# Optimization experiments

Measured on AMD Instinct MI355X. Metric: run time of the kernel, lower is better.

The kernel has to match this reference:

```python
import jax, jax.numpy as jnp
import numpy as np

B, N, DX, DZ = 16384, 128, 5, 2
R_DIAG = 0.1

def setup_inputs() -> dict:
    key = jax.random.key(0)
    ks = jax.random.split(key, 8)
    inp = {
        'state_old': jax.random.normal(ks[0], (B, N, DX), jnp.float32),
        'y': jax.random.normal(ks[1], (B, N, DZ), jnp.float32),
        'encoding': jax.random.normal(ks[2], (B, 128), jnp.float32),
        'pw1': jax.random.normal(ks[3], (2, 16), jnp.float32) * (1.0 / np.sqrt(2.0)),
        'pb1': jnp.zeros((16,), jnp.float32),
        'pw2': jax.random.normal(ks[4], (16, 32), jnp.float32) * (1.0 / np.sqrt(16.0)),
        'pb2': jnp.zeros((32,), jnp.float32),
        'pw3': jax.random.normal(ks[5], (32, 2), jnp.float32) * (1.0 / np.sqrt(32.0)),
        'pb3': jnp.zeros((2,), jnp.float32),
        'nw1': jax.random.normal(ks[6], (128, 32), jnp.float32) * (1.0 / np.sqrt(128.0)),
        'nb1': jnp.zeros((32,), jnp.float32),
        'nw2': jax.random.normal(ks[7], (32, 2), jnp.float32) * (1.0 / np.sqrt(32.0)),
        'nb2': jnp.zeros((2,), jnp.float32),
        # ObservationNoise build(): learned bias init = sqrt(r_diag^2 - 0.001), fixed bias init = 0.001
        'learned_obs_bias': jnp.full((DZ,), float(np.sqrt(R_DIAG**2 - 0.001)), jnp.float32),
        'fixed_obs_bias': jnp.full((DZ,), 0.001, jnp.float32),
    }
    return inp

def _process_model(state, pw1, pb1, pw2, pb2, pw3, pb3):
    # state: [B*N, 5] -> nonlinear unicycle propagation + learned residual on [v, theta_dot]
    theta = state[:, 2] + state[:, 4]
    v = state[:, 3]
    theta_dot = state[:, 4]
    x = state[:, 0] + v * jnp.sin(theta)
    y = state[:, 1] + v * jnp.cos(theta)
    data_in = jnp.stack([v, theta_dot], axis=-1)  # [B*N, 2]
    h = jax.nn.relu(data_in @ pw1 + pb1)
    h = jax.nn.relu(h @ pw2 + pb2)
    data_out = data_in + (h @ pw3 + pb3)
    return jnp.concatenate([x[:, None], y[:, None], theta[:, None], data_out], axis=-1)

def reference(state_old, y, encoding, pw1, pb1, pw2, pb2, pw3, pb3,
              nw1, nb1, nw2, nb2, learned_obs_bias, fixed_obs_bias):
    b, n, dx = state_old.shape
    dz = y.shape[-1]
    # --- predict step: propagate every ensemble member through the process model ---
    Xp = _process_model(state_old.reshape(b * n, dx), pw1, pb1, pw2, pb2, pw3, pb3)
    Xp = Xp.reshape(b, n, dx)
    # --- observation model: H picks state dims 3,4 (H = [[0,0,0,1,0],[0,0,0,0,1]]) ---
    HX = Xp[..., 3:5]  # [b, n, dz]
    # --- observation noise R (heteroscedastic diag) from encoding ---
    d = jax.nn.relu(encoding @ nw1 + nb1) @ nw2 + nb2  # [b, dz]
    diag = jnp.square(d + learned_obs_bias) + fixed_obs_bias
    R = jnp.eye(dz, dtype=diag.dtype) * diag[:, None, :]  # [b, dz, dz]
    # --- ensemble statistics ---
    A = Xp - Xp.mean(axis=1, keepdims=True)    # state anomalies [b, n, dx]
    HA = HX - HX.mean(axis=1, keepdims=True)   # obs anomalies   [b, n, dz]
    denom = jnp.asarray(n - 1, Xp.dtype)
    Pzz = jnp.einsum('bnz,bnw->bzw', HA, HA) / denom + R  # [b, dz, dz]
    Pxz = jnp.einsum('bnx,bnz->bxz', A, HA) / denom       # [b, dx, dz]
    # Kalman gain K = Pxz @ inv(Pzz); compute K^T via batched solve
    Kt = jnp.linalg.solve(Pzz, jnp.swapaxes(Pxz, 1, 2))   # [b, dz, dx]
    innovation = y - HX                                   # [b, n, dz]
    X_new = Xp + jnp.einsum('bnz,bzx->bnx', innovation, Kt)
    return X_new
```

## Files before the change

kernel.cpp:

```cpp
#include <hip/hip_runtime.h>


#define NBPB 4

typedef __bf16 bf16x8 __attribute__((ext_vector_type(8)));
typedef float  f32x16 __attribute__((ext_vector_type(16)));

__global__ __launch_bounds__(256) void ekf_fused(
    const float* __restrict__ state_old,
    const float* __restrict__ y_obs,
    const float* __restrict__ encoding,
    const float* __restrict__ pw1,
    const float* __restrict__ pb1,
    const float* __restrict__ pw2,
    const float* __restrict__ pb2,
    const float* __restrict__ pw3,
    const float* __restrict__ pb3,
    const float* __restrict__ nw1,
    const float* __restrict__ nb1,
    const float* __restrict__ nw2,
    const float* __restrict__ nb2,
    const float* __restrict__ lob,
    const float* __restrict__ fob,
    float* __restrict__ out)
{
    __shared__ __align__(16) float s_state[NBPB * 640];

    const int t = threadIdx.x;
    const int base = blockIdx.x * NBPB;

    {
        const float4* src = (const float4*)(state_old + (size_t)base * 640);
        float4* dst = (float4*)s_state;
        #pragma unroll
        for (int i = t; i < NBPB * 160; i += 256) dst[i] = src[i];
    }
    __syncthreads();

    const int w = t >> 6;
    const int l = t & 63;
    const int c = l & 31;
    const int h = l >> 5;
    const size_t b = (size_t)base + w;

    float diag0, diag1;
    {
        const float4* eg4 = (const float4*)(encoding + b * 128) + h * 16;
        const float* wp = nw1 + (size_t)(h * 64) * 32 + c;
        float a0 = 0.f, a1 = 0.f, a2 = 0.f, a3 = 0.f;
        #pragma unroll
        for (int kk = 0; kk < 16; ++kk) {
            float4 e4 = eg4[kk];
            a0 = fmaf(e4.x, wp[(4 * kk + 0) * 32], a0);
            a1 = fmaf(e4.y, wp[(4 * kk + 1) * 32], a1);
            a2 = fmaf(e4.z, wp[(4 * kk + 2) * 32], a2);
            a3 = fmaf(e4.w, wp[(4 * kk + 3) * 32], a3);
        }
        float acc = (a0 + a1) + (a2 + a3);
        acc += __shfl_xor(acc, 32, 64);
        acc += nb1[c];
        float hh = fmaxf(acc, 0.f);
        float d0 = hh * nw2[2 * c + 0];
        float d1 = hh * nw2[2 * c + 1];
        #pragma unroll
        for (int off = 1; off < 32; off <<= 1) {
            d0 += __shfl_xor(d0, off, 64);
            d1 += __shfl_xor(d1, off, 64);
        }
        float e0 = d0 + nb2[0] + lob[0];
        float e1 = d1 + nb2[1] + lob[1];
        diag0 = fmaf(e0, e0, fob[0]);
        diag1 = fmaf(e1, e1, fob[1]);
    }

    const float4 pw1a0 = *(const float4*)(pw1 + 8 * h);
    const float4 pw1a1 = *(const float4*)(pw1 + 8 * h + 4);
    const float4 pw1b0 = *(const float4*)(pw1 + 16 + 8 * h);
    const float4 pw1b1 = *(const float4*)(pw1 + 16 + 8 * h + 4);
    const float4 pb1k0 = *(const float4*)(pb1 + 8 * h);
    const float4 pb1k1 = *(const float4*)(pb1 + 8 * h + 4);
    float4 pb2v[4], pw3lo[4], pw3hi[4];
    #pragma unroll
    for (int gr = 0; gr < 4; ++gr) {
        pb2v[gr]  = *(const float4*)(pb2 + 8 * gr + 4 * h);
        pw3lo[gr] = *(const float4*)(pw3 + 16 * gr + 8 * h);
        pw3hi[gr] = *(const float4*)(pw3 + 16 * gr + 8 * h + 4);
    }
    bf16x8 afrag;
    #pragma unroll
    for (int q = 0; q < 8; ++q)
        afrag[q] = (__bf16)pw2[(8 * h + q) * 32 + c];
    f32x16 cinit;
    #pragma unroll
    for (int gr = 0; gr < 4; ++gr) {
        cinit[4 * gr + 0] = pb2v[gr].x;
        cinit[4 * gr + 1] = pb2v[gr].y;
        cinit[4 * gr + 2] = pb2v[gr].z;
        cinit[4 * gr + 3] = pb2v[gr].w;
    }

    const float* sp = s_state + w * 640;
    float o3m[4], o4m[4];
    #pragma unroll
    for (int m = 0; m < 4; ++m) {
        const float* s5 = sp + (c + 32 * m) * 5;
        float v = s5[3], td = s5[4];
        bf16x8 bfrag;
        bfrag[0] = (__bf16)fmaxf(0.f, fmaf(v, pw1a0.x, fmaf(td, pw1b0.x, pb1k0.x)));
        bfrag[1] = (__bf16)fmaxf(0.f, fmaf(v, pw1a0.y, fmaf(td, pw1b0.y, pb1k0.y)));
        bfrag[2] = (__bf16)fmaxf(0.f, fmaf(v, pw1a0.z, fmaf(td, pw1b0.z, pb1k0.z)));
        bfrag[3] = (__bf16)fmaxf(0.f, fmaf(v, pw1a0.w, fmaf(td, pw1b0.w, pb1k0.w)));
        bfrag[4] = (__bf16)fmaxf(0.f, fmaf(v, pw1a1.x, fmaf(td, pw1b1.x, pb1k1.x)));
        bfrag[5] = (__bf16)fmaxf(0.f, fmaf(v, pw1a1.y, fmaf(td, pw1b1.y, pb1k1.y)));
        bfrag[6] = (__bf16)fmaxf(0.f, fmaf(v, pw1a1.z, fmaf(td, pw1b1.z, pb1k1.z)));
        bfrag[7] = (__bf16)fmaxf(0.f, fmaf(v, pw1a1.w, fmaf(td, pw1b1.w, pb1k1.w)));
        f32x16 acc = __builtin_amdgcn_mfma_f32_32x32x16_bf16(afrag, bfrag, cinit, 0, 0, 0);
        float o3 = 0.f, o4 = 0.f;
        #pragma unroll
        for (int gr = 0; gr < 4; ++gr) {
            float r0 = fmaxf(acc[4 * gr + 0], 0.f);
            float r1 = fmaxf(acc[4 * gr + 1], 0.f);
            float r2 = fmaxf(acc[4 * gr + 2], 0.f);
            float r3 = fmaxf(acc[4 * gr + 3], 0.f);
            o3 = fmaf(r0, pw3lo[gr].x, o3); o4 = fmaf(r0, pw3lo[gr].y, o4);
            o3 = fmaf(r1, pw3lo[gr].z, o3); o4 = fmaf(r1, pw3lo[gr].w, o4);
            o3 = fmaf(r2, pw3hi[gr].x, o3); o4 = fmaf(r2, pw3hi[gr].y, o4);
            o3 = fmaf(r3, pw3hi[gr].z, o3); o4 = fmaf(r3, pw3hi[gr].w, o4);
        }
        o3m[m] = o3; o4m[m] = o4;
    }
    #pragma unroll
    for (int m = 0; m < 4; ++m) {
        o3m[m] += __shfl_xor(o3m[m], 32, 64);
        o4m[m] += __shfl_xor(o4m[m], 32, 64);
    }

    const float pb30 = pb3[0], pb31 = pb3[1];
    float o3s0 = h ? o3m[2] : o3m[0];
    float o3s1 = h ? o3m[3] : o3m[1];
    float o4s0 = h ? o4m[2] : o4m[0];
    float o4s1 = h ? o4m[3] : o4m[1];
    float xpo[2][5];
    #pragma unroll
    for (int mm = 0; mm < 2; ++mm) {
        const float* s5 = sp + (c + 32 * (2 * h + mm)) * 5;
        float s0 = s5[0], s1 = s5[1], s2 = s5[2], v = s5[3], td = s5[4];
        float th = s2 + td;
        xpo[mm][0] = fmaf(v, __sinf(th), s0);
        xpo[mm][1] = fmaf(v, __cosf(th), s1);
        xpo[mm][2] = th;
        xpo[mm][3] = v  + (mm ? o3s1 : o3s0) + pb30;
        xpo[mm][4] = td + (mm ? o4s1 : o4s0) + pb31;
    }

    float red[14];
    #pragma unroll
    for (int i = 0; i < 5; ++i) red[i] = xpo[0][i] + xpo[1][i];
    red[5]  = xpo[0][0] * xpo[0][3] + xpo[1][0] * xpo[1][3];
    red[6]  = xpo[0][0] * xpo[0][4] + xpo[1][0] * xpo[1][4];
    red[7]  = xpo[0][1] * xpo[0][3] + xpo[1][1] * xpo[1][3];
    red[8]  = xpo[0][1] * xpo[0][4] + xpo[1][1] * xpo[1][4];
    red[9]  = xpo[0][2] * xpo[0][3] + xpo[1][2] * xpo[1][3];
    red[10] = xpo[0][2] * xpo[0][4] + xpo[1][2] * xpo[1][4];
    red[11] = xpo[0][3] * xpo[0][3] + xpo[1][3] * xpo[1][3];
    red[12] = xpo[0][3] * xpo[0][4] + xpo[1][3] * xpo[1][4];
    red[13] = xpo[0][4] * xpo[0][4] + xpo[1][4] * xpo[1][4];
    #pragma unroll
    for (int off = 1; off < 64; off <<= 1) {
        #pragma unroll
        for (int r = 0; r < 14; ++r)
            red[r] += __shfl_xor(red[r], off, 64);
    }

    const float inv  = 1.0f / 127.0f;
    const float minv = inv * 0.0078125f;
    float S00 = red[5]  * inv - red[0] * red[3] * minv;
    float S01 = red[6]  * inv - red[0] * red[4] * minv;
    float S10 = red[7]  * inv - red[1] * red[3] * minv;
    float S11 = red[8]  * inv - red[1] * red[4] * minv;
    float S20 = red[9]  * inv - red[2] * red[3] * minv;
    float S21 = red[10] * inv - red[2] * red[4] * minv;
    float S30 = red[11] * inv - red[3] * red[3] * minv;
    float S31 = red[12] * inv - red[3] * red[4] * minv;
    float S40 = S31;
    float S41 = red[13] * inv - red[4] * red[4] * minv;
    float p00 = S30 + diag0, p01 = S31, p10 = S40, p11 = S41 + diag1;
    float rdet = 1.0f / (p00 * p11 - p01 * p10);
    float Ka0 = (p11 * S00 - p01 * S01) * rdet, Kb0 = (p00 * S01 - p10 * S00) * rdet;
    float Ka1 = (p11 * S10 - p01 * S11) * rdet, Kb1 = (p00 * S11 - p10 * S10) * rdet;
    float Ka2 = (p11 * S20 - p01 * S21) * rdet, Kb2 = (p00 * S21 - p10 * S20) * rdet;
    float Ka3 = (p11 * S30 - p01 * S31) * rdet, Kb3 = (p00 * S31 - p10 * S30) * rdet;
    float Ka4 = (p11 * S40 - p01 * S41) * rdet, Kb4 = (p00 * S41 - p10 * S40) * rdet;

    #pragma unroll
    for (int mm = 0; mm < 2; ++mm) {
        const int p = c + 32 * (2 * h + mm);
        const float2 yy = *(const float2*)(y_obs + (b * 128 + (size_t)p) * 2);
        float i0 = yy.x - xpo[mm][3];
        float i1 = yy.y - xpo[mm][4];
        float* o = out + (b * 128 + (size_t)p) * 5;
        o[0] = xpo[mm][0] + i0 * Ka0 + i1 * Kb0;
        o[1] = xpo[mm][1] + i0 * Ka1 + i1 * Kb1;
        o[2] = xpo[mm][2] + i0 * Ka2 + i1 * Kb2;
        o[3] = xpo[mm][3] + i0 * Ka3 + i1 * Kb3;
        o[4] = xpo[mm][4] + i0 * Ka4 + i1 * Kb4;
    }
}

extern "C" void kernel_launch(void* const* d_in, const int* in_sizes, int n_in,
                              void* d_out, int out_size, void* d_ws, size_t ws_size,
                              hipStream_t stream) {
    const float* state_old = (const float*)d_in[0];
    const float* y_obs     = (const float*)d_in[1];
    const float* encoding  = (const float*)d_in[2];
    const float* pw1 = (const float*)d_in[3];
    const float* pb1 = (const float*)d_in[4];
    const float* pw2 = (const float*)d_in[5];
    const float* pb2 = (const float*)d_in[6];
    const float* pw3 = (const float*)d_in[7];
    const float* pb3 = (const float*)d_in[8];
    const float* nw1 = (const float*)d_in[9];
    const float* nb1 = (const float*)d_in[10];
    const float* nw2 = (const float*)d_in[11];
    const float* nb2 = (const float*)d_in[12];
    const float* lob = (const float*)d_in[13];
    const float* fob = (const float*)d_in[14];
    float* out = (float*)d_out;

    const int B = 16384;
    dim3 grid(B / NBPB);
    dim3 block(256);
    hipLaunchKernelGGL(ekf_fused, grid, block, 0, stream,
                       state_old, y_obs, encoding,
                       pw1, pb1, pw2, pb2, pw3, pb3,
                       nw1, nb1, nw2, nb2, lob, fob, out);
}
```

Before: 43.39 us.

## Replace bf16 MFMA process-model MLP with fp32 FMA using LDS-staged weights

Drops the bf16 MFMA path for the 16x32 hidden layer. Each thread now evaluates the full MLP for its own two ensemble members with scalar fp32 FMAs, reading pw2/pb2/pw3 from a transposed shared-memory table that each block fills. This removes the bf16 conversions, the MFMA setup and the cross-half shuffles, and it restores fp32 accuracy. In exchange each thread does many more VALU FMAs (about 1k per member pair) and reads LDS every iteration, so the cost may go up.

```diff
diff --git a/kernel.cpp b/kernel.cpp
--- a/kernel.cpp
+++ b/kernel.cpp
@@ -2,9 +2,6 @@
 
 
 #define NBPB 4
-
-typedef __bf16 bf16x8 __attribute__((ext_vector_type(8)));
-typedef float  f32x16 __attribute__((ext_vector_type(16)));
 
 __global__ __launch_bounds__(256) void ekf_fused(
     const float* __restrict__ state_old,
@@ -25,6 +22,7 @@
     float* __restrict__ out)
 {
     __shared__ __align__(16) float s_state[NBPB * 640];
+    __shared__ __align__(16) float s_wt[32 * 20];
 
     const int t = threadIdx.x;
     const int base = blockIdx.x * NBPB;
@@ -34,6 +32,16 @@
         float4* dst = (float4*)s_state;
         #pragma unroll
         for (int i = t; i < NBPB * 160; i += 256) dst[i] = src[i];
+        for (int idx = t; idx < 640; idx += 256) {
+            int j = idx / 20, r = idx % 20;
+            float v;
+            if (r < 16)       v = pw2[r * 32 + j];
+            else if (r == 16) v = pb2[j];
+            else if (r == 17) v = pw3[2 * j];
+            else if (r == 18) v = pw3[2 * j + 1];
+            else              v = 0.0f;
+            s_wt[idx] = v;
+        }
     }
     __syncthreads();
 
@@ -73,84 +81,71 @@
         diag1 = fmaf(e1, e1, fob[1]);
     }
 
-    const float4 pw1a0 = *(const float4*)(pw1 + 8 * h);
-    const float4 pw1a1 = *(const float4*)(pw1 + 8 * h + 4);
-    const float4 pw1b0 = *(const float4*)(pw1 + 16 + 8 * h);
-    const float4 pw1b1 = *(const float4*)(pw1 + 16 + 8 * h + 4);
-    const float4 pb1k0 = *(const float4*)(pb1 + 8 * h);
-    const float4 pb1k1 = *(const float4*)(pb1 + 8 * h + 4);
-    float4 pb2v[4], pw3lo[4], pw3hi[4];
-    #pragma unroll
-    for (int gr = 0; gr < 4; ++gr) {
-        pb2v[gr]  = *(const float4*)(pb2 + 8 * gr + 4 * h);
-        pw3lo[gr] = *(const float4*)(pw3 + 16 * gr + 8 * h);
-        pw3hi[gr] = *(const float4*)(pw3 + 16 * gr + 8 * h + 4);
-    }
-    bf16x8 afrag;
-    #pragma unroll
-    for (int q = 0; q < 8; ++q)
-        afrag[q] = (__bf16)pw2[(8 * h + q) * 32 + c];
-    f32x16 cinit;
-    #pragma unroll
-    for (int gr = 0; gr < 4; ++gr) {
-        cinit[4 * gr + 0] = pb2v[gr].x;
-        cinit[4 * gr + 1] = pb2v[gr].y;
-        cinit[4 * gr + 2] = pb2v[gr].z;
-        cinit[4 * gr + 3] = pb2v[gr].w;
-    }
-
     const float* sp = s_state + w * 640;
-    float o3m[4], o4m[4];
-    #pragma unroll
-    for (int m = 0; m < 4; ++m) {
-        const float* s5 = sp + (c + 32 * m) * 5;
-        float v = s5[3], td = s5[4];
-        bf16x8 bfrag;
-        bfrag[0] = (__bf16)fmaxf(0.f, fmaf(v, pw1a0.x, fmaf(td, pw1b0.x, pb1k0.x)));
-        bfrag[1] = (__bf16)fmaxf(0.f, fmaf(v, pw1a0.y, fmaf(td, pw1b0.y, pb1k0.y)));
-        bfrag[2] = (__bf16)fmaxf(0.f, fmaf(v, pw1a0.z, fmaf(td, pw1b0.z, pb1k0.z)));
-        bfrag[3] = (__bf16)fmaxf(0.f, fmaf(v, pw1a0.w, fmaf(td, pw1b0.w, pb1k0.w)));
-        bfrag[4] = (__bf16)fmaxf(0.f, fmaf(v, pw1a1.x, fmaf(td, pw1b1.x, pb1k1.x)));
-        bfrag[5] = (__bf16)fmaxf(0.f, fmaf(v, pw1a1.y, fmaf(td, pw1b1.y, pb1k1.y)));
-        bfrag[6] = (__bf16)fmaxf(0.f, fmaf(v, pw1a1.z, fmaf(td, pw1b1.z, pb1k1.z)));
-        bfrag[7] = (__bf16)fmaxf(0.f, fmaf(v, pw1a1.w, fmaf(td, pw1b1.w, pb1k1.w)));
-        f32x16 acc = __builtin_amdgcn_mfma_f32_32x32x16_bf16(afrag, bfrag, cinit, 0, 0, 0);
-        float o3 = 0.f, o4 = 0.f;
-        #pragma unroll
-        for (int gr = 0; gr < 4; ++gr) {
-            float r0 = fmaxf(acc[4 * gr + 0], 0.f);
-            float r1 = fmaxf(acc[4 * gr + 1], 0.f);
-            float r2 = fmaxf(acc[4 * gr + 2], 0.f);
-            float r3 = fmaxf(acc[4 * gr + 3], 0.f);
-            o3 = fmaf(r0, pw3lo[gr].x, o3); o4 = fmaf(r0, pw3lo[gr].y, o4);
-            o3 = fmaf(r1, pw3lo[gr].z, o3); o4 = fmaf(r1, pw3lo[gr].w, o4);
-            o3 = fmaf(r2, pw3hi[gr].x, o3); o4 = fmaf(r2, pw3hi[gr].y, o4);
-            o3 = fmaf(r3, pw3hi[gr].z, o3); o4 = fmaf(r3, pw3hi[gr].w, o4);
-        }
-        o3m[m] = o3; o4m[m] = o4;
-    }
-    #pragma unroll
-    for (int m = 0; m < 4; ++m) {
-        o3m[m] += __shfl_xor(o3m[m], 32, 64);
-        o4m[m] += __shfl_xor(o4m[m], 32, 64);
-    }
-
-    const float pb30 = pb3[0], pb31 = pb3[1];
-    float o3s0 = h ? o3m[2] : o3m[0];
-    float o3s1 = h ? o3m[3] : o3m[1];
-    float o4s0 = h ? o4m[2] : o4m[0];
-    float o4s1 = h ? o4m[3] : o4m[1];
+    const int p0 = c + 32 * (2 * h);
+    const int p1 = c + 32 * (2 * h + 1);
+
     float xpo[2][5];
-    #pragma unroll
-    for (int mm = 0; mm < 2; ++mm) {
-        const float* s5 = sp + (c + 32 * (2 * h + mm)) * 5;
-        float s0 = s5[0], s1 = s5[1], s2 = s5[2], v = s5[3], td = s5[4];
-        float th = s2 + td;
-        xpo[mm][0] = fmaf(v, __sinf(th), s0);
-        xpo[mm][1] = fmaf(v, __cosf(th), s1);
-        xpo[mm][2] = th;
-        xpo[mm][3] = v  + (mm ? o3s1 : o3s0) + pb30;
-        xpo[mm][4] = td + (mm ? o4s1 : o4s0) + pb31;
+    float va, tda, vb, tdb;
+    {
+        const float* s5a = sp + p0 * 5;
+        const float* s5b = sp + p1 * 5;
+        va = s5a[3]; tda = s5a[4];
+        vb = s5b[3]; tdb = s5b[4];
+        float tha = s5a[2] + tda;
+        float thb = s5b[2] + tdb;
+        xpo[0][0] = fmaf(va, __sinf(tha), s5a[0]);
+        xpo[0][1] = fmaf(va, __cosf(tha), s5a[1]);
+        xpo[0][2] = tha;
+        xpo[1][0] = fmaf(vb, __sinf(thb), s5b[0]);
+        xpo[1][1] = fmaf(vb, __cosf(thb), s5b[1]);
+        xpo[1][2] = thb;
+    }
+    float h1a[16], h1b[16];
+    #pragma unroll
+    for (int q = 0; q < 16; ++q) {
+        float w0 = pw1[q], w1 = pw1[16 + q], bq = pb1[q];
+        h1a[q] = fmaxf(0.f, fmaf(va, w0, fmaf(tda, w1, bq)));
+        h1b[q] = fmaxf(0.f, fmaf(vb, w0, fmaf(tdb, w1, bq)));
+    }
+
+    float o3a = 0.f, o4a = 0.f, o3b = 0.f, o4b = 0.f;
+    #pragma unroll 2
+    for (int j = 0; j < 32; ++j) {
+        const float* wj = s_wt + j * 20;
+        float4 w0 = *(const float4*)(wj);
+        float4 w1 = *(const float4*)(wj + 4);
+        float4 w2 = *(const float4*)(wj + 8);
+        float4 w3 = *(const float4*)(wj + 12);
+        float pb2j = wj[16];
+        float acca = pb2j, accb = pb2j;
+        acca = fmaf(h1a[0],  w0.x, acca); accb = fmaf(h1b[0],  w0.x, accb);
+        acca = fmaf(h1a[1],  w0.y, acca); accb = fmaf(h1b[1],  w0.y, accb);
+        acca = fmaf(h1a[2],  w0.z, acca); accb = fmaf(h1b[2],  w0.z, accb);
+        acca = fmaf(h1a[3],  w0.w, acca); accb = fmaf(h1b[3],  w0.w, accb);
+        acca = fmaf(h1a[4],  w1.x, acca); accb = fmaf(h1b[4],  w1.x, accb);
+        acca = fmaf(h1a[5],  w1.y, acca); accb = fmaf(h1b[5],  w1.y, accb);
+        acca = fmaf(h1a[6],  w1.z, acca); accb = fmaf(h1b[6],  w1.z, accb);
+        acca = fmaf(h1a[7],  w1.w, acca); accb = fmaf(h1b[7],  w1.w, accb);
+        acca = fmaf(h1a[8],  w2.x, acca); accb = fmaf(h1b[8],  w2.x, accb);
+        acca = fmaf(h1a[9],  w2.y, acca); accb = fmaf(h1b[9],  w2.y, accb);
+        acca = fmaf(h1a[10], w2.z, acca); accb = fmaf(h1b[10], w2.z, accb);
+        acca = fmaf(h1a[11], w2.w, acca); accb = fmaf(h1b[11], w2.w, accb);
+        acca = fmaf(h1a[12], w3.x, acca); accb = fmaf(h1b[12], w3.x, accb);
+        acca = fmaf(h1a[13], w3.y, acca); accb = fmaf(h1b[13], w3.y, accb);
+        acca = fmaf(h1a[14], w3.z, acca); accb = fmaf(h1b[14], w3.z, accb);
+        acca = fmaf(h1a[15], w3.w, acca); accb = fmaf(h1b[15], w3.w, accb);
+        float ra = fmaxf(acca, 0.f), rb = fmaxf(accb, 0.f);
+        float w30 = wj[17], w31 = wj[18];
+        o3a = fmaf(ra, w30, o3a); o4a = fmaf(ra, w31, o4a);
+        o3b = fmaf(rb, w30, o3b); o4b = fmaf(rb, w31, o4b);
+    }
+    {
+        float pb30 = pb3[0], pb31 = pb3[1];
+        xpo[0][3] = va + o3a + pb30;
+        xpo[0][4] = tda + o4a + pb31;
+        xpo[1][3] = vb + o3b + pb30;
+        xpo[1][4] = tdb + o4b + pb31;
     }
 
     float red[14];
```

Result: slower. 62.47 us (+44.0%).
